# Optimization experiments

Hardware: AMD Instinct MI355X
Metric: run time of the kernel (lower is better)

Reference implementation:

```python
import jax, jax.numpy as jnp
import numpy as np

BN_EPS = 1e-5


def setup_inputs() -> dict:
    key = jax.random.key(0)
    ks = jax.random.split(key, 8)
    B, C, H, W = 8, 256, 64, 64
    Ci = 128
    x = jax.random.normal(ks[0], (B, C, H, W), dtype=jnp.float32)
    # 1x1 conv weights stored as [out, in] (kernel size 1 squeezed)
    sc = 1.0 / np.sqrt(C)
    g_w = jax.random.uniform(ks[1], (Ci, C), jnp.float32, -sc, sc)
    g_b = jax.random.uniform(ks[2], (Ci,), jnp.float32, -sc, sc)
    theta_w = jax.random.uniform(ks[3], (Ci, C), jnp.float32, -sc, sc)
    theta_b = jax.random.uniform(ks[4], (Ci,), jnp.float32, -sc, sc)
    phi_w = jax.random.uniform(ks[5], (Ci, C), jnp.float32, -sc, sc)
    phi_b = jax.random.uniform(ks[6], (Ci,), jnp.float32, -sc, sc)
    # W conv: normal(std=0.01) weight, zero bias (per _init_weights)
    W_w = 0.01 * jax.random.normal(ks[7], (C, Ci), dtype=jnp.float32)
    W_b = jnp.zeros((C,), dtype=jnp.float32)
    bn_gamma = jnp.ones((C,), dtype=jnp.float32)
    bn_beta = jnp.zeros((C,), dtype=jnp.float32)
    return {"x": x, "g_w": g_w, "g_b": g_b, "theta_w": theta_w, "theta_b": theta_b,
            "phi_w": phi_w, "phi_b": phi_b, "W_w": W_w, "W_b": W_b,
            "bn_gamma": bn_gamma, "bn_beta": bn_beta}


def reference(x, g_w, g_b, theta_w, theta_b, phi_w, phi_b, W_w, W_b, bn_gamma, bn_beta):
    B, C, H, W = x.shape
    xf = x.reshape(B, C, H * W)                                   # [B, C, N]
    # 1x1 convs == per-position channel GEMMs
    g_x = jnp.einsum('oc,bcn->bon', g_w, xf) + g_b[:, None]        # [B, Ci, N]
    th = jnp.einsum('oc,bcn->bon', theta_w, xf) + theta_b[:, None]
    ph = jnp.einsum('oc,bcn->bon', phi_w, xf) + phi_b[:, None]
    # theta^T phi : [B, N, N] dense attention scores
    f = jnp.einsum('bcn,bcm->bnm', th, ph)
    attn = jax.nn.softmax(f, axis=-1)
    # attention-weighted sum of g values -> [B, Ci, N]
    y = jnp.einsum('bnm,bcm->bcn', attn, g_x)
    # output 1x1 conv + BatchNorm2d (training-mode batch stats)
    wy = jnp.einsum('oc,bcn->bon', W_w, y) + W_b[:, None]          # [B, C, N]
    mean = jnp.mean(wy, axis=(0, 2), keepdims=True)
    var = jnp.var(wy, axis=(0, 2), keepdims=True)
    wy_bn = (wy - mean) * jax.lax.rsqrt(var + BN_EPS)
    wy_bn = wy_bn * bn_gamma[:, None] + bn_beta[:, None]
    z = wy_bn.reshape(B, C, H, W) + x
    return z
```

## Files before the change

kernel.cpp:

```cpp
#include <hip/hip_runtime.h>
#include <hip/hip_bf16.h>
#include <math.h>

#define B_   8
#define C_   256
#define CI_  128
#define N_   4096

typedef unsigned short ushort_t;
typedef unsigned int uint_t;
typedef __attribute__((ext_vector_type(8))) short short8;
typedef __attribute__((ext_vector_type(16))) float floatx16;
typedef __attribute__((ext_vector_type(2))) unsigned int uint2v;

#define OFF_W3B  0ull
#define OFF_B3   196608ull
#define OFF_WCB  198144ull
#define OFF_XT   263680ull
#define OFF_THT  17040896ull
#define OFF_PHT  25429504ull
#define OFF_G16  33818112ull
#define OFF_LP   42206720ull
#define OFF_YPB  42468864ull
#define OFF_WY   263680ull
#define OFF_ST   59246080ull

__device__ __forceinline__ ushort_t f2bf(float x) {
  union { float f; uint_t u; } c; c.f = x;
  return (ushort_t)((c.u + 0x7fffu + ((c.u >> 16) & 1u)) >> 16);
}
__device__ __forceinline__ uint_t pkbf(float a, float b) {
  __hip_bfloat162 h = __float22bfloat162_rn(float2{a, b});
  union { __hip_bfloat162 h; uint_t u; } c; c.h = h; return c.u;
}
__device__ __forceinline__ float bf_lo(uint_t u) {
  union { uint_t u; float f; } c; c.u = u << 16; return c.f;
}
__device__ __forceinline__ float bf_hi(uint_t u) {
  union { uint_t u; float f; } c; c.u = u & 0xffff0000u; return c.f;
}
__device__ __forceinline__ float fexp2(float x) {
  float r; asm("v_exp_f32 %0, %1\ns_nop 0" : "=v"(r) : "v"(x)); return r;
}
__device__ __forceinline__ void async_copy16(const void* g, void* l) {
  __builtin_amdgcn_global_load_lds(
      (const __attribute__((address_space(1))) unsigned int*)g,
      (__attribute__((address_space(3))) unsigned int*)l, 16, 0, 0);
}

__global__ __launch_bounds__(256) void pack_w(
    const float* __restrict__ g_w, const float* __restrict__ g_b,
    const float* __restrict__ th_w, const float* __restrict__ th_b,
    const float* __restrict__ ph_w, const float* __restrict__ ph_b,
    const float* __restrict__ W_w,
    ushort_t* __restrict__ W3b, float* __restrict__ b3,
    ushort_t* __restrict__ Wc, float* __restrict__ st)
{
  int bid = blockIdx.x;
  if (bid < 384) {
    int i = bid * 256 + threadIdx.x;
    int o = i >> 8;
    float v;
    if (o < 128)      v = g_w[i];
    else if (o < 256) v = th_w[i - 128*256];
    else              v = ph_w[i - 256*256];
    W3b[i] = f2bf(v);
    if ((i & 255) == 0)
      b3[o] = (o < 128) ? g_b[o] : (o < 256) ? th_b[o - 128] : ph_b[o - 256];
  } else if (bid < 512) {
    int j = (bid - 384) * 256 + threadIdx.x;
    Wc[j] = f2bf(W_w[j]);
  } else {
    st[threadIdx.x] = 0.f;
    st[256 + threadIdx.x] = 0.f;
  }
}

__global__ __launch_bounds__(256) void xcast(
    const float* __restrict__ x, ushort_t* __restrict__ xt)
{
  const int b = blockIdx.z, c0 = blockIdx.y * 64, n0 = blockIdx.x * 64;
  const int tid = threadIdx.x;
  __shared__ float xs[64][65];
  const int nq = (tid & 15) * 4, cr = tid >> 4;
  #pragma unroll
  for (int i = 0; i < 4; ++i) {
    float4 v = *(const float4*)&x[((size_t)b * C_ + c0 + cr + 16*i) * N_ + n0 + nq];
    xs[cr + 16*i][nq] = v.x; xs[cr + 16*i][nq+1] = v.y;
    xs[cr + 16*i][nq+2] = v.z; xs[cr + 16*i][nq+3] = v.w;
  }
  __syncthreads();
  const int n = tid >> 2, cs = (tid & 3) * 16;
  uint_t u[8];
  #pragma unroll
  for (int j = 0; j < 8; ++j)
    u[j] = pkbf(xs[cs + 2*j][n], xs[cs + 2*j + 1][n]);
  ushort_t* dst = &xt[((size_t)b * N_ + n0 + n) * C_ + c0 + cs];
  *(uint4*)dst       = make_uint4(u[0], u[1], u[2], u[3]);
  *(uint4*)(dst + 8) = make_uint4(u[4], u[5], u[6], u[7]);
}

__global__ __launch_bounds__(256, 2) void proj_all(
    const ushort_t* __restrict__ W3b, const float* __restrict__ b3,
    const ushort_t* __restrict__ xt, ushort_t* __restrict__ tht,
    ushort_t* __restrict__ pht, ushort_t* __restrict__ g16)
{
  const int b = blockIdx.z, nb = blockIdx.x, ot = blockIdx.y;
  const int gm = (ot == 2);
  const int o0 = gm ? 0 : (128 + ot * 128);
  const int tid = threadIdx.x, w = tid >> 6, lane = tid & 63;
  const int l31 = lane & 31, h = lane >> 5, xk = l31 & 7;
  __shared__ ushort_t ws_l[2 * 128 * 64];
  __shared__ ushort_t xs_l[2 * 128 * 64];
  const ushort_t* xb = xt + (size_t)b * N_ * C_;
  const int n0 = nb * 128;
  floatx16 acc[4];
  #pragma unroll
  for (int ct = 0; ct < 4; ++ct)
    #pragma unroll
    for (int r = 0; r < 16; ++r) acc[ct][r] = 0.f;

  const int gr = lane >> 3, gu = lane & 7;

  #define PSTAGE(k0v, bufv)                                                   \
    {                                                                         \
      ushort_t* wsb = ws_l + (bufv) * 8192;                                   \
      ushort_t* xsb = xs_l + (bufv) * 8192;                                   \
      _Pragma("unroll")                                                       \
      for (int i = 0; i < 4; ++i) {                                           \
        int r = w*32 + i*8 + gr;                                              \
        async_copy16(&W3b[(size_t)(o0 + r) * C_ + (k0v) + ((gu ^ (r & 7)) * 8)], \
                     &wsb[(w*32 + i*8) * 64]);                                \
        async_copy16(&xb[(size_t)(n0 + r) * C_ + (k0v) + ((gu ^ (r & 7)) * 8)],  \
                     &xsb[(w*32 + i*8) * 64]);                                \
      }                                                                       \
    }

  PSTAGE(0, 0);
  asm volatile("s_waitcnt vmcnt(0)" ::: "memory");
  __builtin_amdgcn_s_barrier();

  for (int kt = 0; kt < 4; ++kt) {
    const int cur = kt & 1;
    if (kt < 3) PSTAGE((kt + 1) * 64, cur ^ 1);
    const ushort_t* wsb = ws_l + cur * 8192;
    const ushort_t* xsb = xs_l + cur * 8192;
    const ushort_t* bmat = gm ? wsb : xsb;
    const ushort_t* amat = gm ? xsb : wsb;
    #pragma unroll
    for (int kk = 0; kk < 4; ++kk) {
      int fc = ((2*kk + h) ^ xk) * 8;
      short8 bf = *(const short8*)&bmat[(w*32 + l31) * 64 + fc];
      #pragma unroll
      for (int ct = 0; ct < 4; ++ct) {
        short8 af = *(const short8*)&amat[(ct*32 + l31) * 64 + fc];
        acc[ct] = __builtin_amdgcn_mfma_f32_32x32x16_bf16(af, bf, acc[ct], 0, 0, 0);
      }
    }
    asm volatile("s_waitcnt vmcnt(0)" ::: "memory");
    __builtin_amdgcn_s_barrier();
  }

  if (gm) {
    float bv = b3[w*32 + l31];
    ushort_t* gp = g16 + ((size_t)b * CI_ + w*32 + l31) * N_;
    #pragma unroll
    for (int ct = 0; ct < 4; ++ct)
      #pragma unroll
      for (int rq = 0; rq < 4; ++rq) {
        uint2 d = make_uint2(pkbf(acc[ct][4*rq+0] + bv, acc[ct][4*rq+1] + bv),
                             pkbf(acc[ct][4*rq+2] + bv, acc[ct][4*rq+3] + bv));
        *(uint2*)&gp[n0 + ct*32 + 8*rq + 4*h] = d;
      }
  } else {
    ushort_t* tp = ((ot == 0) ? tht : pht) + ((size_t)b * N_ + n0 + w*32 + l31) * CI_;
    #pragma unroll
    for (int ct = 0; ct < 4; ++ct)
      #pragma unroll
      for (int rq = 0; rq < 4; ++rq) {
        float4 bv = *(const float4*)&b3[o0 + ct*32 + 8*rq + 4*h];
        uint2 d = make_uint2(pkbf(acc[ct][4*rq+0] + bv.x, acc[ct][4*rq+1] + bv.y),
                             pkbf(acc[ct][4*rq+2] + bv.z, acc[ct][4*rq+3] + bv.w));
        *(uint2*)&tp[ct*32 + 8*rq + 4*h] = d;
      }
  }
}

#define LOG2E_  1.442695041f
#define MBIAS_  (-28.85390082f)

__global__ __launch_bounds__(256, 3) void attn_mfma(
    const ushort_t* __restrict__ tht, const ushort_t* __restrict__ pht,
    const ushort_t* __restrict__ g16, ushort_t* __restrict__ yp,
    float* __restrict__ lp)
{
  const int b  = blockIdx.x & 7;
  const int ms = (blockIdx.x >> 3) & 1;
  const int qb = blockIdx.x >> 4;
  const int tid = threadIdx.x, w = tid >> 6, lane = tid & 63;
  const int l31 = lane & 31, h = lane >> 5, xk = l31 & 7;

  __shared__ ushort_t smem[24576];

  const int q0w = qb * 128 + w * 32;
  const int m_base = ms * 2048;

  const ushort_t* thb = tht + (size_t)b * N_ * CI_;
  const ushort_t* phb = pht + (size_t)b * N_ * CI_;
  const ushort_t* gbp = g16 + (size_t)b * CI_ * N_;

  short8 tf[8];
  #pragma unroll
  for (int kk = 0; kk < 8; ++kk)
    tf[kk] = *(const short8*)&thb[(size_t)(q0w + l31) * CI_ + kk*16 + h*8];

  floatx16 acc[4];
  #pragma unroll
  for (int ct = 0; ct < 4; ++ct)
    #pragma unroll
    for (int r = 0; r < 16; ++r) acc[ct][r] = 0.f;
  float lpart = 0.f;

  const int phr = lane >> 4, phu = lane & 15;
  const int gr  = lane >> 3, gu  = lane & 7;

  #define STAGE_PHS(m0v, bufv)                                                \
    {                                                                         \
      ushort_t* phs_ = smem + (bufv) * 8192;                                  \
      _Pragma("unroll")                                                       \
      for (int i = 0; i < 4; ++i) {                                           \
        int row = w*16 + i*4 + phr;                                           \
        async_copy16(&phb[(size_t)((m0v) + row) * CI_ + ((phu ^ (row & 7)) * 8)], \
                     &phs_[(w*16 + i*4) * 128]);                              \
      }                                                                       \
    }
  #define STAGE_GS(m0v)                                                       \
    {                                                                         \
      ushort_t* gs_ = smem + 16384;                                           \
      _Pragma("unroll")                                                       \
      for (int i = 0; i < 4; ++i) {                                           \
        int c = w*32 + i*8 + gr;                                              \
        async_copy16(&gbp[(size_t)c * N_ + (m0v) + ((gu ^ (c & 7)) * 8)],     \
                     &gs_[(w*32 + i*8) * 64]);                                \
      }                                                                       \
    }

  #define SMPV(sv, mtv)                                                       \
    {                                                                         \
      uint_t Aw[4], Bw[4];                                                    \
      float ls = 0.f;                                                         \
      _Pragma("unroll")                                                       \
      for (int rq = 0; rq < 4; ++rq) {                                        \
        float p0 = fexp2(fmaf(sv[4*rq+0], LOG2E_, MBIAS_));                   \
        float p1 = fexp2(fmaf(sv[4*rq+1], LOG2E_, MBIAS_));                   \
        float p2 = fexp2(fmaf(sv[4*rq+2], LOG2E_, MBIAS_));                   \
        float p3 = fexp2(fmaf(sv[4*rq+3], LOG2E_, MBIAS_));                   \
        ls += (p0 + p1) + (p2 + p3);                                          \
        Aw[rq] = pkbf(p0, p1);                                                \
        Bw[rq] = pkbf(p2, p3);                                                \
      }                                                                       \
      lpart += ls;                                                            \
      _Pragma("unroll")                                                       \
      for (int t = 0; t < 2; ++t) {                                           \
        uint2v ra = __builtin_amdgcn_permlane32_swap(Aw[2*t], Aw[2*t+1], false, false); \
        uint2v rb = __builtin_amdgcn_permlane32_swap(Bw[2*t], Bw[2*t+1], false, false); \
        union { uint_t u[4]; short8 s; } pk_;                                 \
        pk_.u[0] = ra.x; pk_.u[1] = rb.x; pk_.u[2] = ra.y; pk_.u[3] = rb.y;   \
        const int pc = ((2*(2*(mtv) + t) + h) ^ xk) * 8;                      \
        __builtin_amdgcn_s_setprio(1);                                        \
        _Pragma("unroll")                                                     \
        for (int ct = 0; ct < 4; ++ct) {                                      \
          short8 gf = *(const short8*)&gs[(ct*32 + l31) * 64 + pc];           \
          acc[ct] = __builtin_amdgcn_mfma_f32_32x32x16_bf16(gf, pk_.s, acc[ct], 0, 0, 0); \
        }                                                                     \
        __builtin_amdgcn_s_setprio(0);                                        \
      }                                                                       \
    }

  const ushort_t* gs = smem + 16384;

  STAGE_PHS(m_base, 0);
  asm volatile("s_waitcnt vmcnt(0)" ::: "memory");
  __builtin_amdgcn_s_barrier();

  for (int it = 0; it < 32; ++it) {
    const int cur = it & 1;
    const int m0 = m_base + it * 64;
    STAGE_GS(m0);
    if (it < 31) STAGE_PHS(m0 + 64, cur ^ 1);
    const ushort_t* phs = smem + cur * 8192;

    floatx16 s;
    #pragma unroll
    for (int r = 0; r < 16; ++r) s[r] = 0.f;
    __builtin_amdgcn_s_setprio(1);
    #pragma unroll
    for (int kk = 0; kk < 8; ++kk) {
      short8 pf = *(const short8*)&phs[l31 * 128 + (((2*kk + h) ^ xk) * 8)];
      s = __builtin_amdgcn_mfma_f32_32x32x16_bf16(pf, tf[kk], s, 0, 0, 0);
    }
    __builtin_amdgcn_s_setprio(0);

    if (it < 31) { asm volatile("s_waitcnt vmcnt(4)" ::: "memory"); }
    else         { asm volatile("s_waitcnt vmcnt(0)" ::: "memory"); }
    __builtin_amdgcn_s_barrier();

    SMPV(s, 0)

    #pragma unroll
    for (int r = 0; r < 16; ++r) s[r] = 0.f;
    __builtin_amdgcn_s_setprio(1);
    #pragma unroll
    for (int kk = 0; kk < 8; ++kk) {
      short8 pf = *(const short8*)&phs[(32 + l31) * 128 + (((2*kk + h) ^ xk) * 8)];
      s = __builtin_amdgcn_mfma_f32_32x32x16_bf16(pf, tf[kk], s, 0, 0, 0);
    }
    __builtin_amdgcn_s_setprio(0);

    SMPV(s, 1)

    asm volatile("s_waitcnt vmcnt(0)" ::: "memory");
    __builtin_amdgcn_s_barrier();
  }

  float lq = lpart + __shfl_xor(lpart, 32);
  if (h == 0)
    lp[((size_t)ms * 8 + b) * N_ + q0w + l31] = lq;

  __syncthreads();
  ushort_t* tr = smem + w * 4096;
  #pragma unroll
  for (int ct = 0; ct < 4; ++ct)
    #pragma unroll
    for (int rq = 0; rq < 4; ++rq) {
      uint2 d = make_uint2(pkbf(acc[ct][4*rq+0], acc[ct][4*rq+1]),
                           pkbf(acc[ct][4*rq+2], acc[ct][4*rq+3]));
      *(uint2*)&tr[l31 * 128 + ct*32 + 8*rq + 4*h] = d;
    }
  ushort_t* ypb = yp + (((size_t)ms * 8 + b) * N_ + q0w) * CI_;
  #pragma unroll
  for (int itx = 0; itx < 8; ++itx) {
    int row = itx*4 + (lane >> 4);
    int cu  = (lane & 15) * 8;
    uint4 v = *(const uint4*)&tr[row * 128 + cu];
    *(uint4*)&ypb[(size_t)row * CI_ + cu] = v;
  }
}

__global__ __launch_bounds__(256, 2) void wgemm_fused(
    const ushort_t* __restrict__ Wc, const float* __restrict__ Wb,
    const ushort_t* __restrict__ yp, const float* __restrict__ lp,
    ushort_t* __restrict__ WYb)
{
  const int b = blockIdx.z, nb = blockIdx.x, ot = blockIdx.y;
  const int o0 = ot * 128;
  const int tid = threadIdx.x, w = tid >> 6, lane = tid & 63;
  const int l31 = lane & 31, h = lane >> 5, xk = l31 & 7;
  __shared__ ushort_t ws_l[128 * 128];
  __shared__ ushort_t xs_l[128 * 128];
  const int n0 = nb * 128;
  const size_t PH = (size_t)B_ * N_ * CI_;
  const ushort_t* yp0 = yp + (size_t)b * N_ * CI_;
  const ushort_t* yp1 = yp0 + PH;
  floatx16 acc[4];
  #pragma unroll
  for (int ct = 0; ct < 4; ++ct)
    #pragma unroll
    for (int r = 0; r < 16; ++r) acc[ct][r] = 0.f;

  const int rr = lane >> 4;
  const int uu = lane & 15;

  #pragma unroll
  for (int i = 0; i < 8; ++i) {
    int r = w*32 + i*4 + rr;
    async_copy16(&Wc[(size_t)(o0 + r) * CI_ + ((uu ^ (r & 7)) * 8)],
                 &ws_l[(w*32 + i*4) * 128]);
  }
  #pragma unroll
  for (int i = 0; i < 8; ++i) {
    int rl = w*32 + i*4 + rr;
    int n = n0 + rl;
    size_t src = (size_t)n * CI_ + ((uu ^ (rl & 7)) * 8);
    uint4 a0 = *(const uint4*)&yp0[src];
    uint4 a1 = *(const uint4*)&yp1[src];
    float inv = 1.0f / (lp[(size_t)b * N_ + n] + lp[(size_t)(8 + b) * N_ + n]);
    uint4 o;
    o.x = pkbf((bf_lo(a0.x) + bf_lo(a1.x)) * inv, (bf_hi(a0.x) + bf_hi(a1.x)) * inv);
    o.y = pkbf((bf_lo(a0.y) + bf_lo(a1.y)) * inv, (bf_hi(a0.y) + bf_hi(a1.y)) * inv);
    o.z = pkbf((bf_lo(a0.z) + bf_lo(a1.z)) * inv, (bf_hi(a0.z) + bf_hi(a1.z)) * inv);
    o.w = pkbf((bf_lo(a0.w) + bf_lo(a1.w)) * inv, (bf_hi(a0.w) + bf_hi(a1.w)) * inv);
    *(uint4*)&xs_l[rl * 128 + uu * 8] = o;
  }
  __syncthreads();

  #pragma unroll
  for (int kk = 0; kk < 8; ++kk) {
    int fc = ((2*kk + h) ^ xk) * 8;
    short8 bf = *(const short8*)&xs_l[(w*32 + l31) * 128 + fc];
    #pragma unroll
    for (int ct = 0; ct < 4; ++ct) {
      short8 af = *(const short8*)&ws_l[(ct*32 + l31) * 128 + fc];
      acc[ct] = __builtin_amdgcn_mfma_f32_32x32x16_bf16(af, bf, acc[ct], 0, 0, 0);
    }
  }

  const int n = n0 + w*32 + l31;
  #pragma unroll
  for (int ct = 0; ct < 4; ++ct)
    #pragma unroll
    for (int rq = 0; rq < 4; ++rq) {
      float4 bv = *(const float4*)&Wb[o0 + ct*32 + 8*rq + 4*h];
      #pragma unroll
      for (int j = 0; j < 4; ++j) {
        int o = o0 + ct*32 + 8*rq + 4*h + j;
        WYb[((size_t)b * C_ + o) * N_ + n] = f2bf(acc[ct][4*rq + j] + (&bv.x)[j]);
      }
    }
}

__global__ __launch_bounds__(256) void bn_stats(
    const ushort_t* __restrict__ WYb, float* __restrict__ st)
{
  const int o  = blockIdx.x & 255;
  const int bb = blockIdx.x >> 8;
  const int tid = threadIdx.x;
  const ushort_t* p = WYb + ((size_t)bb * C_ + o) * N_;
  float s = 0.f, s2 = 0.f;
  #pragma unroll
  for (int j = 0; j < 2; ++j) {
    uint4 v = *(const uint4*)&p[tid * 16 + j * 8];
    float f0 = bf_lo(v.x), f1 = bf_hi(v.x), f2 = bf_lo(v.y), f3 = bf_hi(v.y);
    float f4 = bf_lo(v.z), f5 = bf_hi(v.z), f6 = bf_lo(v.w), f7 = bf_hi(v.w);
    s  += ((f0 + f1) + (f2 + f3)) + ((f4 + f5) + (f6 + f7));
    s2 += ((f0*f0 + f1*f1) + (f2*f2 + f3*f3)) + ((f4*f4 + f5*f5) + (f6*f6 + f7*f7));
  }
  #pragma unroll
  for (int m = 32; m >= 1; m >>= 1) {
    s  += __shfl_xor(s, m);
    s2 += __shfl_xor(s2, m);
  }
  __shared__ float rs[8];
  const int w = tid >> 6, lane = tid & 63;
  if (lane == 0) { rs[w] = s; rs[4 + w] = s2; }
  __syncthreads();
  if (tid == 0) {
    atomicAdd(&st[o],       (rs[0] + rs[1]) + (rs[2] + rs[3]));
    atomicAdd(&st[256 + o], (rs[4] + rs[5]) + (rs[6] + rs[7]));
  }
}

__global__ __launch_bounds__(256) void bn_apply(
    const ushort_t* __restrict__ WYb, const float* __restrict__ x,
    const float* __restrict__ st, const float* __restrict__ gamma,
    const float* __restrict__ beta, float* __restrict__ out)
{
  size_t i = ((size_t)blockIdx.x * 256 + threadIdx.x) * 4;
  int o = (int)((i >> 12) & 255);
  uint2 wv = *(const uint2*)&WYb[i];
  float4 xv = *(const float4*)&x[i];
  const float invM = 1.0f / (float)(B_ * N_);
  float mean = st[o] * invM;
  float var  = st[256 + o] * invM - mean * mean;
  float gsc = gamma[o] * rsqrtf(var + 1e-5f);
  float bb  = beta[o] - mean * gsc;
  float4 v;
  v.x = bf_lo(wv.x) * gsc + bb + xv.x;
  v.y = bf_hi(wv.x) * gsc + bb + xv.y;
  v.z = bf_lo(wv.y) * gsc + bb + xv.z;
  v.w = bf_hi(wv.y) * gsc + bb + xv.w;
  *(float4*)&out[i] = v;
}

extern "C" void kernel_launch(void* const* d_in, const int* in_sizes, int n_in,
                              void* d_out, int out_size, void* d_ws, size_t ws_size,
                              hipStream_t stream)
{
  const float* x       = (const float*)d_in[0];
  const float* g_w     = (const float*)d_in[1];
  const float* g_b     = (const float*)d_in[2];
  const float* theta_w = (const float*)d_in[3];
  const float* theta_b = (const float*)d_in[4];
  const float* phi_w   = (const float*)d_in[5];
  const float* phi_b   = (const float*)d_in[6];
  const float* W_w     = (const float*)d_in[7];
  const float* W_b     = (const float*)d_in[8];
  const float* gamma   = (const float*)d_in[9];
  const float* beta    = (const float*)d_in[10];
  float* out = (float*)d_out;

  char* ws = (char*)d_ws;
  ushort_t* W3b = (ushort_t*)(ws + OFF_W3B);
  float*    b3  = (float*)(ws + OFF_B3);
  ushort_t* Wc  = (ushort_t*)(ws + OFF_WCB);
  ushort_t* xt  = (ushort_t*)(ws + OFF_XT);
  ushort_t* tht = (ushort_t*)(ws + OFF_THT);
  ushort_t* pht = (ushort_t*)(ws + OFF_PHT);
  ushort_t* g16 = (ushort_t*)(ws + OFF_G16);
  float*    lpp = (float*)(ws + OFF_LP);
  ushort_t* ypb = (ushort_t*)(ws + OFF_YPB);
  ushort_t* WYb = (ushort_t*)(ws + OFF_WY);
  float*    ST  = (float*)(ws + OFF_ST);

  pack_w<<<513, 256, 0, stream>>>(g_w, g_b, theta_w, theta_b, phi_w, phi_b,
                                  W_w, W3b, b3, Wc, ST);
  xcast<<<dim3(64, 4, 8), 256, 0, stream>>>(x, xt);
  proj_all<<<dim3(32, 3, 8), 256, 0, stream>>>(W3b, b3, xt, tht, pht, g16);
  attn_mfma<<<512, 256, 0, stream>>>(tht, pht, g16, ypb, lpp);
  wgemm_fused<<<dim3(32, 2, 8), 256, 0, stream>>>(Wc, W_b, ypb, lpp, WYb);
  bn_stats<<<2048, 256, 0, stream>>>(WYb, ST);
  bn_apply<<<8192, 256, 0, stream>>>(WYb, x, ST, gamma, beta, out);
}
```

Before: 228.4 us.

## Split attention key range four ways and combine partial sums via atomics

The attention kernel now splits the key dimension into four chunks instead of two, doubling the grid to 1024 blocks with half the loop iterations each. Row sums are accumulated with atomicAdd into a zeroed buffer, and the four partial outputs are summed in the output GEMM prologue. The workspace layout is rearranged so the extra partial buffers overlap the dead xt region. This is meant to improve occupancy and load balance across CUs, at the cost of more partial-output traffic and extra loads in the combine step.

Result: slower. 234.3 us (+2.6%).

```diff
diff --git a/kernel.cpp b/kernel.cpp
--- a/kernel.cpp
+++ b/kernel.cpp
@@ -13,17 +13,18 @@
 typedef __attribute__((ext_vector_type(16))) float floatx16;
 typedef __attribute__((ext_vector_type(2))) unsigned int uint2v;
 
-#define OFF_W3B  0ull
-#define OFF_B3   196608ull
-#define OFF_WCB  198144ull
-#define OFF_XT   263680ull
-#define OFF_THT  17040896ull
-#define OFF_PHT  25429504ull
-#define OFF_G16  33818112ull
-#define OFF_LP   42206720ull
-#define OFF_YPB  42468864ull
-#define OFF_WY   263680ull
-#define OFF_ST   59246080ull
+#define OFF_W3B   0ull
+#define OFF_B3    196608ull
+#define OFF_WCB   198144ull
+#define OFF_LP    263680ull
+#define OFF_ST    394752ull
+#define OFF_THT   396800ull
+#define OFF_PHT   8785408ull
+#define OFF_G16   17174016ull
+#define OFF_XT    25562624ull
+#define OFF_YP23  25562624ull
+#define OFF_YP01  42339840ull
+#define OFF_WY    396800ull
 
 __device__ __forceinline__ ushort_t f2bf(float x) {
   union { float f; uint_t u; } c; c.f = x;
@@ -54,7 +55,8 @@
     const float* __restrict__ ph_w, const float* __restrict__ ph_b,
     const float* __restrict__ W_w,
     ushort_t* __restrict__ W3b, float* __restrict__ b3,
-    ushort_t* __restrict__ Wc, float* __restrict__ st)
+    ushort_t* __restrict__ Wc, float* __restrict__ st,
+    float* __restrict__ lp)
 {
   int bid = blockIdx.x;
   if (bid < 384) {
@@ -70,9 +72,11 @@
   } else if (bid < 512) {
     int j = (bid - 384) * 256 + threadIdx.x;
     Wc[j] = f2bf(W_w[j]);
-  } else {
+  } else if (bid == 512) {
     st[threadIdx.x] = 0.f;
     st[256 + threadIdx.x] = 0.f;
+  } else {
+    lp[(bid - 513) * 256 + threadIdx.x] = 0.f;
   }
 }
 
@@ -191,19 +195,19 @@
 
 __global__ __launch_bounds__(256, 3) void attn_mfma(
     const ushort_t* __restrict__ tht, const ushort_t* __restrict__ pht,
-    const ushort_t* __restrict__ g16, ushort_t* __restrict__ yp,
-    float* __restrict__ lp)
+    const ushort_t* __restrict__ g16, ushort_t* __restrict__ ypA,
+    ushort_t* __restrict__ ypB, float* __restrict__ lp)
 {
   const int b  = blockIdx.x & 7;
-  const int ms = (blockIdx.x >> 3) & 1;
-  const int qb = blockIdx.x >> 4;
+  const int ms = (blockIdx.x >> 3) & 3;
+  const int qb = blockIdx.x >> 5;
   const int tid = threadIdx.x, w = tid >> 6, lane = tid & 63;
   const int l31 = lane & 31, h = lane >> 5, xk = l31 & 7;
 
   __shared__ ushort_t smem[24576];
 
   const int q0w = qb * 128 + w * 32;
-  const int m_base = ms * 2048;
+  const int m_base = ms * 1024;
 
   const ushort_t* thb = tht + (size_t)b * N_ * CI_;
   const ushort_t* phb = pht + (size_t)b * N_ * CI_;
@@ -283,11 +287,11 @@
   asm volatile("s_waitcnt vmcnt(0)" ::: "memory");
   __builtin_amdgcn_s_barrier();
 
-  for (int it = 0; it < 32; ++it) {
+  for (int it = 0; it < 16; ++it) {
     const int cur = it & 1;
     const int m0 = m_base + it * 64;
     STAGE_GS(m0);
-    if (it < 31) STAGE_PHS(m0 + 64, cur ^ 1);
+    if (it < 15) STAGE_PHS(m0 + 64, cur ^ 1);
     const ushort_t* phs = smem + cur * 8192;
 
     floatx16 s;
@@ -301,7 +305,7 @@
     }
     __builtin_amdgcn_s_setprio(0);
 
-    if (it < 31) { asm volatile("s_waitcnt vmcnt(4)" ::: "memory"); }
+    if (it < 15) { asm volatile("s_waitcnt vmcnt(4)" ::: "memory"); }
     else         { asm volatile("s_waitcnt vmcnt(0)" ::: "memory"); }
     __builtin_amdgcn_s_barrier();
 
@@ -325,7 +329,7 @@
 
   float lq = lpart + __shfl_xor(lpart, 32);
   if (h == 0)
-    lp[((size_t)ms * 8 + b) * N_ + q0w + l31] = lq;
+    atomicAdd(&lp[(size_t)b * N_ + q0w + l31], lq);
 
   __syncthreads();
   ushort_t* tr = smem + w * 4096;
@@ -337,7 +341,8 @@
                            pkbf(acc[ct][4*rq+2], acc[ct][4*rq+3]));
       *(uint2*)&tr[l31 * 128 + ct*32 + 8*rq + 4*h] = d;
     }
-  ushort_t* ypb = yp + (((size_t)ms * 8 + b) * N_ + q0w) * CI_;
+  ushort_t* ypb = ((ms < 2) ? ypA : ypB)
+                + (((size_t)(ms & 1) * B_ + b) * N_ + q0w) * CI_;
   #pragma unroll
   for (int itx = 0; itx < 8; ++itx) {
     int row = itx*4 + (lane >> 4);
@@ -349,8 +354,8 @@
 
 __global__ __launch_bounds__(256, 2) void wgemm_fused(
     const ushort_t* __restrict__ Wc, const float* __restrict__ Wb,
-    const ushort_t* __restrict__ yp, const float* __restrict__ lp,
-    ushort_t* __restrict__ WYb)
+    const ushort_t* __restrict__ ypA, const ushort_t* __restrict__ ypB,
+    const float* __restrict__ lp, ushort_t* __restrict__ WYb)
 {
   const int b = blockIdx.z, nb = blockIdx.x, ot = blockIdx.y;
   const int o0 = ot * 128;
@@ -360,8 +365,10 @@
   __shared__ ushort_t xs_l[128 * 128];
   const int n0 = nb * 128;
   const size_t PH = (size_t)B_ * N_ * CI_;
-  const ushort_t* yp0 = yp + (size_t)b * N_ * CI_;
+  const ushort_t* yp0 = ypA + (size_t)b * N_ * CI_;
   const ushort_t* yp1 = yp0 + PH;
+  const ushort_t* yp2 = ypB + (size_t)b * N_ * CI_;
+  const ushort_t* yp3 = yp2 + PH;
   floatx16 acc[4];
   #pragma unroll
   for (int ct = 0; ct < 4; ++ct)
@@ -384,12 +391,18 @@
     size_t src = (size_t)n * CI_ + ((uu ^ (rl & 7)) * 8);
     uint4 a0 = *(const uint4*)&yp0[src];
     uint4 a1 = *(const uint4*)&yp1[src];
-    float inv = 1.0f / (lp[(size_t)b * N_ + n] + lp[(size_t)(8 + b) * N_ + n]);
+    uint4 a2 = *(const uint4*)&yp2[src];
+    uint4 a3 = *(const uint4*)&yp3[src];
+    float inv = 1.0f / lp[(size_t)b * N_ + n];
     uint4 o;
-    o.x = pkbf((bf_lo(a0.x) + bf_lo(a1.x)) * inv, (bf_hi(a0.x) + bf_hi(a1.x)) * inv);
-    o.y = pkbf((bf_lo(a0.y) + bf_lo(a1.y)) * inv, (bf_hi(a0.y) + bf_hi(a1.y)) * inv);
-    o.z = pkbf((bf_lo(a0.z) + bf_lo(a1.z)) * inv, (bf_hi(a0.z) + bf_hi(a1.z)) * inv);
-    o.w = pkbf((bf_lo(a0.w) + bf_lo(a1.w)) * inv, (bf_hi(a0.w) + bf_hi(a1.w)) * inv);
+    o.x = pkbf((bf_lo(a0.x)+bf_lo(a1.x)+bf_lo(a2.x)+bf_lo(a3.x)) * inv,
+               (bf_hi(a0.x)+bf_hi(a1.x)+bf_hi(a2.x)+bf_hi(a3.x)) * inv);
+    o.y = pkbf((bf_lo(a0.y)+bf_lo(a1.y)+bf_lo(a2.y)+bf_lo(a3.y)) * inv,
+               (bf_hi(a0.y)+bf_hi(a1.y)+bf_hi(a2.y)+bf_hi(a3.y)) * inv);
+    o.z = pkbf((bf_lo(a0.z)+bf_lo(a1.z)+bf_lo(a2.z)+bf_lo(a3.z)) * inv,
+               (bf_hi(a0.z)+bf_hi(a1.z)+bf_hi(a2.z)+bf_hi(a3.z)) * inv);
+    o.w = pkbf((bf_lo(a0.w)+bf_lo(a1.w)+bf_lo(a2.w)+bf_lo(a3.w)) * inv,
+               (bf_hi(a0.w)+bf_hi(a1.w)+bf_hi(a2.w)+bf_hi(a3.w)) * inv);
     *(uint4*)&xs_l[rl * 128 + uu * 8] = o;
   }
   __syncthreads();
@@ -493,21 +506,22 @@
   ushort_t* W3b = (ushort_t*)(ws + OFF_W3B);
   float*    b3  = (float*)(ws + OFF_B3);
   ushort_t* Wc  = (ushort_t*)(ws + OFF_WCB);
-  ushort_t* xt  = (ushort_t*)(ws + OFF_XT);
+  float*    lpp = (float*)(ws + OFF_LP);
+  float*    ST  = (float*)(ws + OFF_ST);
   ushort_t* tht = (ushort_t*)(ws + OFF_THT);
   ushort_t* pht = (ushort_t*)(ws + OFF_PHT);
   ushort_t* g16 = (ushort_t*)(ws + OFF_G16);
-  float*    lpp = (float*)(ws + OFF_LP);
-  ushort_t* ypb = (ushort_t*)(ws + OFF_YPB);
+  ushort_t* xt  = (ushort_t*)(ws + OFF_XT);
+  ushort_t* ypA = (ushort_t*)(ws + OFF_YP01);
+  ushort_t* ypB = (ushort_t*)(ws + OFF_YP23);
   ushort_t* WYb = (ushort_t*)(ws + OFF_WY);
-  float*    ST  = (float*)(ws + OFF_ST);
-
-  pack_w<<<513, 256, 0, stream>>>(g_w, g_b, theta_w, theta_b, phi_w, phi_b,
-                                  W_w, W3b, b3, Wc, ST);
+
+  pack_w<<<641, 256, 0, stream>>>(g_w, g_b, theta_w, theta_b, phi_w, phi_b,
+                                  W_w, W3b, b3, Wc, ST, lpp);
   xcast<<<dim3(64, 4, 8), 256, 0, stream>>>(x, xt);
   proj_all<<<dim3(32, 3, 8), 256, 0, stream>>>(W3b, b3, xt, tht, pht, g16);
-  attn_mfma<<<512, 256, 0, stream>>>(tht, pht, g16, ypb, lpp);
-  wgemm_fused<<<dim3(32, 2, 8), 256, 0, stream>>>(Wc, W_b, ypb, lpp, WYb);
+  attn_mfma<<<1024, 256, 0, stream>>>(tht, pht, g16, ypA, ypB, lpp);
+  wgemm_fused<<<dim3(32, 2, 8), 256, 0, stream>>>(Wc, W_b, ypA, ypB, lpp, WYb);
   bn_stats<<<2048, 256, 0, stream>>>(WYb, ST);
   bn_apply<<<8192, 256, 0, stream>>>(WYb, x, ST, gamma, beta, out);
 }
```

## Fuse BN statistics into output GEMM epilogue and merge pack/cast kernels

Applied to the files above, without the earlier changes.

Removes the separate bn_stats kernel: the W-conv GEMM epilogue now reduces sum and sum-of-squares per channel with wave shuffles and atomically adds them into the stats buffer. The weight pack and x transpose/cast kernels are merged into a single launch. This saves two kernel launches and a full re-read of the bf16 WY tensor, but adds many shuffles and far more contended float atomics in the GEMM epilogue.

Result: slower. 592.4 us (+159.3%).

```diff
diff --git a/kernel.cpp b/kernel.cpp
--- a/kernel.cpp
+++ b/kernel.cpp
@@ -48,17 +48,20 @@
       (__attribute__((address_space(3))) unsigned int*)l, 16, 0, 0);
 }
 
-__global__ __launch_bounds__(256) void pack_w(
+__global__ __launch_bounds__(256) void pack_xcast(
     const float* __restrict__ g_w, const float* __restrict__ g_b,
     const float* __restrict__ th_w, const float* __restrict__ th_b,
     const float* __restrict__ ph_w, const float* __restrict__ ph_b,
-    const float* __restrict__ W_w,
+    const float* __restrict__ W_w, const float* __restrict__ x,
     ushort_t* __restrict__ W3b, float* __restrict__ b3,
-    ushort_t* __restrict__ Wc, float* __restrict__ st)
-{
-  int bid = blockIdx.x;
+    ushort_t* __restrict__ Wc, float* __restrict__ st,
+    ushort_t* __restrict__ xt)
+{
+  const int bid = blockIdx.x;
+  const int tid = threadIdx.x;
+  __shared__ float xs[64][65];
   if (bid < 384) {
-    int i = bid * 256 + threadIdx.x;
+    int i = bid * 256 + tid;
     int o = i >> 8;
     float v;
     if (o < 128)      v = g_w[i];
@@ -67,21 +70,19 @@
     W3b[i] = f2bf(v);
     if ((i & 255) == 0)
       b3[o] = (o < 128) ? g_b[o] : (o < 256) ? th_b[o - 128] : ph_b[o - 256];
+    return;
   } else if (bid < 512) {
-    int j = (bid - 384) * 256 + threadIdx.x;
+    int j = (bid - 384) * 256 + tid;
     Wc[j] = f2bf(W_w[j]);
-  } else {
-    st[threadIdx.x] = 0.f;
-    st[256 + threadIdx.x] = 0.f;
-  }
-}
-
-__global__ __launch_bounds__(256) void xcast(
-    const float* __restrict__ x, ushort_t* __restrict__ xt)
-{
-  const int b = blockIdx.z, c0 = blockIdx.y * 64, n0 = blockIdx.x * 64;
-  const int tid = threadIdx.x;
-  __shared__ float xs[64][65];
+    return;
+  } else if (bid == 512) {
+    st[tid] = 0.f;
+    st[256 + tid] = 0.f;
+    return;
+  }
+  const int idx = bid - 513;
+  const int b = idx >> 8, cb = (idx >> 6) & 3, nb = idx & 63;
+  const int c0 = cb * 64, n0 = nb * 64;
   const int nq = (tid & 15) * 4, cr = tid >> 4;
   #pragma unroll
   for (int i = 0; i < 4; ++i) {
@@ -350,7 +351,7 @@
 __global__ __launch_bounds__(256, 2) void wgemm_fused(
     const ushort_t* __restrict__ Wc, const float* __restrict__ Wb,
     const ushort_t* __restrict__ yp, const float* __restrict__ lp,
-    ushort_t* __restrict__ WYb)
+    ushort_t* __restrict__ WYb, float* __restrict__ st)
 {
   const int b = blockIdx.z, nb = blockIdx.x, ot = blockIdx.y;
   const int o0 = ot * 128;
@@ -414,40 +415,20 @@
       #pragma unroll
       for (int j = 0; j < 4; ++j) {
         int o = o0 + ct*32 + 8*rq + 4*h + j;
-        WYb[((size_t)b * C_ + o) * N_ + n] = f2bf(acc[ct][4*rq + j] + (&bv.x)[j]);
+        float v = acc[ct][4*rq + j] + (&bv.x)[j];
+        WYb[((size_t)b * C_ + o) * N_ + n] = f2bf(v);
+        float s = v, s2 = v * v;
+        #pragma unroll
+        for (int m = 16; m >= 1; m >>= 1) {
+          s  += __shfl_xor(s, m);
+          s2 += __shfl_xor(s2, m);
+        }
+        if (l31 == 0) {
+          atomicAdd(&st[o], s);
+          atomicAdd(&st[256 + o], s2);
+        }
       }
     }
-}
-
-__global__ __launch_bounds__(256) void bn_stats(
-    const ushort_t* __restrict__ WYb, float* __restrict__ st)
-{
-  const int o  = blockIdx.x & 255;
-  const int bb = blockIdx.x >> 8;
-  const int tid = threadIdx.x;
-  const ushort_t* p = WYb + ((size_t)bb * C_ + o) * N_;
-  float s = 0.f, s2 = 0.f;
-  #pragma unroll
-  for (int j = 0; j < 2; ++j) {
-    uint4 v = *(const uint4*)&p[tid * 16 + j * 8];
-    float f0 = bf_lo(v.x), f1 = bf_hi(v.x), f2 = bf_lo(v.y), f3 = bf_hi(v.y);
-    float f4 = bf_lo(v.z), f5 = bf_hi(v.z), f6 = bf_lo(v.w), f7 = bf_hi(v.w);
-    s  += ((f0 + f1) + (f2 + f3)) + ((f4 + f5) + (f6 + f7));
-    s2 += ((f0*f0 + f1*f1) + (f2*f2 + f3*f3)) + ((f4*f4 + f5*f5) + (f6*f6 + f7*f7));
-  }
-  #pragma unroll
-  for (int m = 32; m >= 1; m >>= 1) {
-    s  += __shfl_xor(s, m);
-    s2 += __shfl_xor(s2, m);
-  }
-  __shared__ float rs[8];
-  const int w = tid >> 6, lane = tid & 63;
-  if (lane == 0) { rs[w] = s; rs[4 + w] = s2; }
-  __syncthreads();
-  if (tid == 0) {
-    atomicAdd(&st[o],       (rs[0] + rs[1]) + (rs[2] + rs[3]));
-    atomicAdd(&st[256 + o], (rs[4] + rs[5]) + (rs[6] + rs[7]));
-  }
 }
 
 __global__ __launch_bounds__(256) void bn_apply(
@@ -502,12 +483,10 @@
   ushort_t* WYb = (ushort_t*)(ws + OFF_WY);
   float*    ST  = (float*)(ws + OFF_ST);
 
-  pack_w<<<513, 256, 0, stream>>>(g_w, g_b, theta_w, theta_b, phi_w, phi_b,
-                                  W_w, W3b, b3, Wc, ST);
-  xcast<<<dim3(64, 4, 8), 256, 0, stream>>>(x, xt);
+  pack_xcast<<<2561, 256, 0, stream>>>(g_w, g_b, theta_w, theta_b, phi_w,
+                                       phi_b, W_w, x, W3b, b3, Wc, ST, xt);
   proj_all<<<dim3(32, 3, 8), 256, 0, stream>>>(W3b, b3, xt, tht, pht, g16);
   attn_mfma<<<512, 256, 0, stream>>>(tht, pht, g16, ypb, lpp);
-  wgemm_fused<<<dim3(32, 2, 8), 256, 0, stream>>>(Wc, W_b, ypb, lpp, WYb);
-  bn_stats<<<2048, 256, 0, stream>>>(WYb, ST);
+  wgemm_fused<<<dim3(32, 2, 8), 256, 0, stream>>>(Wc, W_b, ypb, lpp, WYb, ST);
   bn_apply<<<8192, 256, 0, stream>>>(WYb, x, ST, gamma, beta, out);
 }
```
